# Kernel optimization log

Measured on AMD Instinct MI355X. Metric: run time of the kernel, lower is better.

Reference implementation:

```python
import jax, jax.numpy as jnp
import numpy as np
from math import pi

K_MAX = 0.1   # init k
DLT_K = 0.02  # init dk
EPS = 0.1

N_IMG, N_ATOM = 32, 400000


def _dot(a, b):
    # sum over last two dims, keepdims -> shape [..., 1, 1]
    return jnp.sum(a * b, axis=(-2, -1), keepdims=True)


def _norm(a):
    return jnp.sqrt(_dot(a, a))


def setup_inputs() -> dict:
    key = jax.random.key(0)
    k1, k2, k3 = jax.random.split(key, 3)
    pos = jax.random.normal(k1, (N_IMG, N_ATOM, 3), dtype=jnp.float32)
    frc = jax.random.normal(k2, (N_IMG, N_ATOM, 3), dtype=jnp.float32)
    eng = jax.random.normal(k3, (N_IMG,), dtype=jnp.float32)
    # ensure climbing-image argmax lies in the interior (valid frc_para index)
    eng = eng.at[N_IMG // 2].add(10.0)
    return {"pos": pos, "frc": frc, "eng": eng}


def reference(pos, frc, eng):
    dtype = pos.dtype
    eng3 = eng[:, None, None]  # [N,1,1]

    # ---- spring force k per segment: [N-1,1,1] ----
    eng_ref = jnp.min(eng3) - EPS
    eng_max = jnp.max(eng3)
    eng_i = jnp.maximum(eng3[1:], eng3[:-1])
    k = K_MAX - DLT_K * (eng_max - eng_i) / (eng_max - eng_ref)
    k = jnp.where(eng_i < eng_ref, K_MAX - DLT_K, k)

    # ---- improved tangent estimation: [N-2, A, 3] ----
    tau_p = pos[1:-1] - pos[:-2]
    tau_m = pos[2:] - pos[1:-1]
    e0, e1, e2 = eng3[:-2], eng3[1:-1], eng3[2:]
    msk_pp = ((e2 > e1) & (e1 > e0)).astype(dtype)
    msk_mm = ((e2 < e1) & (e1 < e0)).astype(dtype)
    not_both = 1.0 - jnp.maximum(msk_pp, msk_mm)
    msk_p = (e2 > e1).astype(dtype) * not_both
    msk_m = (e2 < e1).astype(dtype) * not_both
    dv_max = jnp.maximum(jnp.abs(e2 - e1), jnp.abs(e0 - e1))
    dv_min = jnp.minimum(jnp.abs(e2 - e1), jnp.abs(e0 - e1))
    tau = (tau_p * msk_pp + tau_m * msk_mm
           + (tau_p * dv_max + tau_m * dv_min) * msk_p
           + (tau_p * dv_min + tau_m * dv_max) * msk_m)
    tau = tau / _norm(tau)

    # ---- NEB force decomposition ----
    frc_in = frc[1:-1]
    vecp = pos[2:] - pos[1:-1]
    vecm = pos[1:-1] - pos[:-2]
    frc_para = _dot(frc_in, tau) * tau
    spr = k[1:] * vecp - k[:-1] * vecm
    spr_para = (k[1:] * _norm(vecp) - k[:-1] * _norm(vecm)) * tau
    frc_perp = frc_in - frc_para  # uses pre-climbing frc_para (torch in-place order)
    spr_perp = spr - spr_para

    # climbing image: double parallel force at the highest-energy image
    i = jnp.argmax(eng) - 1  # eng index -> frc_para index offset (interior images)
    # torch indexes frc_para with the raw eng argmax; reproduce that indexing
    i_raw = jnp.argmax(eng)
    frc_para = frc_para.at[i_raw].multiply(2.0)

    frc_neb = spr_para - frc_para  # nudged=True

    # doubly nudged switch term
    sw = (2.0 / pi) * jnp.arctan2(_dot(frc_perp, frc_perp), _dot(spr_perp, spr_perp))
    doubly = spr_perp - _dot(spr_perp, frc_perp) * frc_perp * sw
    frc_neb = frc_neb + doubly

    out_frc = frc + jnp.pad(frc_neb, ((1, 1), (0, 0), (0, 0)))
    return out_frc
```

## Files before the change

### kernel.cpp

```cpp
#include <hip/hip_runtime.h>
#include <math.h>

#define N_IMG 32
#define N_ATOM 400000
#define NE (N_ATOM*3)
#define NE4 (NE/4)
#define KMAXC 0.1f
#define DLTKC 0.02f
#define EPSE 0.1f

#define OFF_SDD 0
#define OFF_SPM 31
#define OFF_SFP 61
#define OFF_SFM 91
#define OFF_SFF 121
#define NSUM 151
#define OFF_CO 160

__device__ __forceinline__ float dot4(float4 a, float4 b) {
    return a.x*b.x + a.y*b.y + a.z*b.z + a.w*b.w;
}
__device__ __forceinline__ float4 sub4(float4 a, float4 b) {
    return make_float4(a.x-b.x, a.y-b.y, a.z-b.z, a.w-b.w);
}

__device__ __forceinline__ float wred_dpp(float x) {
    x += __int_as_float(__builtin_amdgcn_update_dpp(0, __float_as_int(x), 0x111, 0xf, 0xf, false));
    x += __int_as_float(__builtin_amdgcn_update_dpp(0, __float_as_int(x), 0x112, 0xf, 0xf, false));
    x += __int_as_float(__builtin_amdgcn_update_dpp(0, __float_as_int(x), 0x114, 0xf, 0xf, false));
    x += __int_as_float(__builtin_amdgcn_update_dpp(0, __float_as_int(x), 0x118, 0xf, 0xf, false));
    x += __int_as_float(__builtin_amdgcn_update_dpp(0, __float_as_int(x), 0x142, 0xa, 0xf, false));
    x += __int_as_float(__builtin_amdgcn_update_dpp(0, __float_as_int(x), 0x143, 0xc, 0xf, false));
    return x;
}

__global__ __launch_bounds__(256) void eb_pass1(const float* __restrict__ pos,
                                                const float* __restrict__ frc,
                                                float* __restrict__ sums) {
    __shared__ float ls[NSUM];
    for (int i = threadIdx.x; i < NSUM; i += 256) ls[i] = 0.f;
    __syncthreads();

    const int t = blockIdx.x * 256 + threadIdx.x;
    const bool act = t < NE4;
    const float4* pos4 = reinterpret_cast<const float4*>(pos);
    const float4* frc4 = reinterpret_cast<const float4*>(frc);
    const float4 z4 = make_float4(0.f, 0.f, 0.f, 0.f);
    const int lane = threadIdx.x & 63;

    float4 p0 = act ? pos4[t] : z4;
    float4 p1 = act ? pos4[(size_t)NE4 + t] : z4;
    float4 d_prev = sub4(p1, p0);
    {
        float sdd = wred_dpp(dot4(d_prev, d_prev));
        if (lane == 63) atomicAdd(&ls[OFF_SDD + 0], sdd);
    }
    float4 p_prev = p1;

#pragma unroll 5
    for (int r = 2; r < N_IMG; ++r) {
        float4 p = act ? pos4[(size_t)r * NE4 + t] : z4;
        float4 f = act ? frc4[(size_t)(r - 1) * NE4 + t] : z4;
        float4 d = sub4(p, p_prev);
        float sdd = wred_dpp(dot4(d, d));
        float spm = wred_dpp(dot4(d_prev, d));
        float sfp = wred_dpp(dot4(f, d_prev));
        float sfm = wred_dpp(dot4(f, d));
        float sff = wred_dpp(dot4(f, f));
        if (lane == 63) {
            int jj = r - 2;
            atomicAdd(&ls[OFF_SDD + (r - 1)], sdd);
            atomicAdd(&ls[OFF_SPM + jj], spm);
            atomicAdd(&ls[OFF_SFP + jj], sfp);
            atomicAdd(&ls[OFF_SFM + jj], sfm);
            atomicAdd(&ls[OFF_SFF + jj], sff);
        }
        p_prev = p;
        d_prev = d;
    }
    __syncthreads();
    for (int i = threadIdx.x; i < NSUM; i += 256) atomicAdd(&sums[i], ls[i]);
}

__global__ void eb_coeff(const float* __restrict__ eng,
                         const float* __restrict__ sums,
                         float* __restrict__ co) {
    const int jj = threadIdx.x;
    if (jj >= N_IMG - 2 || blockIdx.x != 0) return;
    float e[N_IMG];
    float emin = 1e30f, emax = -1e30f;
    int imax = 0;
    for (int i = 0; i < N_IMG; ++i) {
        float v = eng[i];
        e[i] = v;
        if (v < emin) emin = v;
        if (v > emax) { emax = v; imax = i; }
    }
    const float eref = emin - EPSE;
    float e0 = e[jj], e1 = e[jj + 1], e2 = e[jj + 2];
    float eim = fmaxf(e1, e0);
    float km = KMAXC - DLTKC * (emax - eim) / (emax - eref);
    if (eim < eref) km = KMAXC - DLTKC;
    float eip = fmaxf(e2, e1);
    float kp = KMAXC - DLTKC * (emax - eip) / (emax - eref);
    if (eip < eref) kp = KMAXC - DLTKC;

    float pp = (e2 > e1 && e1 > e0) ? 1.f : 0.f;
    float mm = (e2 < e1 && e1 < e0) ? 1.f : 0.f;
    float nb = 1.f - fmaxf(pp, mm);
    float mp = ((e2 > e1) ? 1.f : 0.f) * nb;
    float mq = ((e2 < e1) ? 1.f : 0.f) * nb;
    float dvmax = fmaxf(fabsf(e2 - e1), fabsf(e0 - e1));
    float dvmin = fminf(fabsf(e2 - e1), fabsf(e0 - e1));
    float a = pp + dvmax * mp + dvmin * mq;
    float b = mm + dvmin * mp + dvmax * mq;
    float Spp = sums[OFF_SDD + jj];
    float Smm = sums[OFF_SDD + jj + 1];
    float Spm = sums[OFF_SPM + jj];
    float Sfp = sums[OFF_SFP + jj];
    float Sfm = sums[OFF_SFM + jj];
    float Sff = sums[OFF_SFF + jj];
    float ntau2 = a * a * Spp + 2.f * a * b * Spm + b * b * Smm;
    float ntau = sqrtf(ntau2);
    float ta = a / ntau, tb = b / ntau;
    float fpar = ta * Sfp + tb * Sfm;
    float spar = kp * sqrtf(Smm) - km * sqrtf(Spp);
    float ffpp = Sff - fpar * fpar;
    float strau = ta * (kp * Spm - km * Spp) + tb * (kp * Smm - km * Spm);
    float Sss = kp * kp * Smm - 2.f * kp * km * Spm + km * km * Spp;
    float sspp = Sss - 2.f * spar * strau + spar * spar;
    float Ssf = kp * Sfm - km * Sfp;
    float spfp = Ssf - fpar * strau;
    float sw = (2.0f / 3.14159265358979323846f) * atan2f(ffpp, sspp);
    float c = spfp * sw;
    float g = (jj == imax) ? 2.f : 1.f;
    float w = (c - g) * fpar / ntau;
    co[jj]      = 1.f - c;
    co[30 + jj] = kp + w * b;
    co[60 + jj] = w * a - km;
}

__global__ __launch_bounds__(256) void eb_pass2(const float* __restrict__ pos,
                                                const float* __restrict__ frc,
                                                const float* __restrict__ co,
                                                float* __restrict__ out) {
    __shared__ float A[30], B[30], C[30];
    if (threadIdx.x < 30) {
        A[threadIdx.x] = co[threadIdx.x];
        B[threadIdx.x] = co[30 + threadIdx.x];
        C[threadIdx.x] = co[60 + threadIdx.x];
    }
    __syncthreads();
    const int t = blockIdx.x * 256 + threadIdx.x;
    if (t >= NE4) return;
    const float4* pos4 = reinterpret_cast<const float4*>(pos);
    const float4* frc4 = reinterpret_cast<const float4*>(frc);
    float4* out4 = reinterpret_cast<float4*>(out);

    size_t i31 = (size_t)31 * NE4 + t;
    float4 p_next = pos4[i31];
    out4[i31] = frc4[i31];
    float4 p30 = pos4[(size_t)30 * NE4 + t];
    float4 d_next = sub4(p_next, p30);
    p_next = p30;
#pragma unroll 5
    for (int l = 29; l >= 0; --l) {
        float4 p = pos4[(size_t)l * NE4 + t];
        float4 d = sub4(p_next, p);
        float4 f = frc4[(size_t)(l + 1) * NE4 + t];
        float ca = A[l], cb = B[l], cc = C[l];
        float4 o;
        o.x = ca * f.x + cb * d_next.x + cc * d.x;
        o.y = ca * f.y + cb * d_next.y + cc * d.y;
        o.z = ca * f.z + cb * d_next.z + cc * d.z;
        o.w = ca * f.w + cb * d_next.w + cc * d.w;
        out4[(size_t)(l + 1) * NE4 + t] = o;
        d_next = d;
        p_next = p;
    }
    out4[t] = frc4[t];
}

extern "C" void kernel_launch(void* const* d_in, const int* in_sizes, int n_in,
                              void* d_out, int out_size, void* d_ws, size_t ws_size,
                              hipStream_t stream) {
    const float* pos = (const float*)d_in[0];
    const float* frc = (const float*)d_in[1];
    const float* eng = (const float*)d_in[2];
    float* out = (float*)d_out;
    float* ws = (float*)d_ws;

    hipMemsetAsync(d_ws, 0, NSUM * sizeof(float), stream);
    const int blocks = (NE4 + 255) / 256;
    eb_pass1<<<blocks, 256, 0, stream>>>(pos, frc, ws);
    eb_coeff<<<1, 64, 0, stream>>>(eng, ws, ws + OFF_CO);
    eb_pass2<<<blocks, 256, 0, stream>>>(pos, frc, ws + OFF_CO, out);
}
```

Baseline: 440.3 us.

## Split image chain into chunks and replace atomic reductions with register partials

The first pass now splits the 30 interior images into 5 chunks spread over a 2D grid. Each thread grid-strides over elements and accumulates all dot-product sums in registers, so the per-image wave reductions and shared/global atomics are gone. Partial sums per block go to a workspace and a new reduce kernel combines them, which also removes the memset. The second pass is likewise chunked over images for more parallelism, at the cost of re-reading one boundary position image per chunk and one extra kernel launch.

```diff
diff --git a/kernel.cpp b/kernel.cpp
--- a/kernel.cpp
+++ b/kernel.cpp
@@ -15,7 +15,13 @@
 #define OFF_SFM 91
 #define OFF_SFF 121
 #define NSUM 151
-#define OFF_CO 160
+#define OFF_CO  160
+#define OFF_PART 256
+#define PSTRIDE 160
+
+#define NBXP 586
+#define NBX2 1172
+#define NCHUNK 5
 
 __device__ __forceinline__ float dot4(float4 a, float4 b) {
     return a.x*b.x + a.y*b.y + a.z*b.z + a.w*b.w;
@@ -36,50 +42,80 @@
 
 __global__ __launch_bounds__(256) void eb_pass1(const float* __restrict__ pos,
                                                 const float* __restrict__ frc,
-                                                float* __restrict__ sums) {
-    __shared__ float ls[NSUM];
-    for (int i = threadIdx.x; i < NSUM; i += 256) ls[i] = 0.f;
-    __syncthreads();
-
-    const int t = blockIdx.x * 256 + threadIdx.x;
-    const bool act = t < NE4;
+                                                float* __restrict__ part) {
+    const int c = blockIdx.y;
+    const int j0 = 1 + 6 * c;
     const float4* pos4 = reinterpret_cast<const float4*>(pos);
     const float4* frc4 = reinterpret_cast<const float4*>(frc);
-    const float4 z4 = make_float4(0.f, 0.f, 0.f, 0.f);
+
+    float sdd[7], spm[6], sfp[6], sfm[6], sff[6];
+#pragma unroll
+    for (int i = 0; i < 7; ++i) sdd[i] = 0.f;
+#pragma unroll
+    for (int i = 0; i < 6; ++i) { spm[i] = 0.f; sfp[i] = 0.f; sfm[i] = 0.f; sff[i] = 0.f; }
+
+    for (int t = blockIdx.x * 256 + threadIdx.x; t < NE4; t += 256 * NBXP) {
+        float4 p_cur = pos4[(size_t)(j0 - 1) * NE4 + t];
+        float4 p_nxt = pos4[(size_t)j0 * NE4 + t];
+        float4 dprev = sub4(p_nxt, p_cur);
+        sdd[0] += dot4(dprev, dprev);
+#pragma unroll
+        for (int jj = 0; jj < 6; ++jj) {
+            const int j = j0 + jj;
+            float4 p2 = pos4[(size_t)(j + 1) * NE4 + t];
+            float4 f  = frc4[(size_t)j * NE4 + t];
+            float4 d  = sub4(p2, p_nxt);
+            sdd[jj + 1] += dot4(d, d);
+            spm[jj] += dot4(dprev, d);
+            sfp[jj] += dot4(f, dprev);
+            sfm[jj] += dot4(f, d);
+            sff[jj] += dot4(f, f);
+            dprev = d;
+            p_nxt = p2;
+        }
+    }
+
+    float v[31];
+#pragma unroll
+    for (int i = 0; i < 7; ++i) v[i] = sdd[i];
+#pragma unroll
+    for (int i = 0; i < 6; ++i) { v[7 + i] = spm[i]; v[13 + i] = sfp[i]; v[19 + i] = sfm[i]; v[25 + i] = sff[i]; }
+
+    __shared__ float red[4][31];
+    const int wave = threadIdx.x >> 6;
     const int lane = threadIdx.x & 63;
-
-    float4 p0 = act ? pos4[t] : z4;
-    float4 p1 = act ? pos4[(size_t)NE4 + t] : z4;
-    float4 d_prev = sub4(p1, p0);
-    {
-        float sdd = wred_dpp(dot4(d_prev, d_prev));
-        if (lane == 63) atomicAdd(&ls[OFF_SDD + 0], sdd);
-    }
-    float4 p_prev = p1;
-
-#pragma unroll 5
-    for (int r = 2; r < N_IMG; ++r) {
-        float4 p = act ? pos4[(size_t)r * NE4 + t] : z4;
-        float4 f = act ? frc4[(size_t)(r - 1) * NE4 + t] : z4;
-        float4 d = sub4(p, p_prev);
-        float sdd = wred_dpp(dot4(d, d));
-        float spm = wred_dpp(dot4(d_prev, d));
-        float sfp = wred_dpp(dot4(f, d_prev));
-        float sfm = wred_dpp(dot4(f, d));
-        float sff = wred_dpp(dot4(f, f));
-        if (lane == 63) {
-            int jj = r - 2;
-            atomicAdd(&ls[OFF_SDD + (r - 1)], sdd);
-            atomicAdd(&ls[OFF_SPM + jj], spm);
-            atomicAdd(&ls[OFF_SFP + jj], sfp);
-            atomicAdd(&ls[OFF_SFM + jj], sfm);
-            atomicAdd(&ls[OFF_SFF + jj], sff);
-        }
-        p_prev = p;
-        d_prev = d;
+#pragma unroll
+    for (int s = 0; s < 31; ++s) {
+        float r = wred_dpp(v[s]);
+        if (lane == 63) red[wave][s] = r;
     }
     __syncthreads();
-    for (int i = threadIdx.x; i < NSUM; i += 256) atomicAdd(&sums[i], ls[i]);
+    const int s = threadIdx.x;
+    if (s < 31) {
+        float r = red[0][s] + red[1][s] + red[2][s] + red[3][s];
+        int slot; bool owned = true;
+        if (s < 7)       { owned = (s < 6) || (c == NCHUNK - 1); slot = OFF_SDD + (j0 - 1) + s; }
+        else if (s < 13) slot = OFF_SPM + (j0 - 1) + (s - 7);
+        else if (s < 19) slot = OFF_SFP + (j0 - 1) + (s - 13);
+        else if (s < 25) slot = OFF_SFM + (j0 - 1) + (s - 19);
+        else             slot = OFF_SFF + (j0 - 1) + (s - 25);
+        if (owned) part[(size_t)blockIdx.x * PSTRIDE + slot] = r;
+    }
+}
+
+__global__ __launch_bounds__(256) void eb_reduce(const float* __restrict__ part,
+                                                 float* __restrict__ sums) {
+    const int s = blockIdx.x;
+    float acc = 0.f;
+    for (int r = threadIdx.x; r < NBXP; r += 256)
+        acc += part[(size_t)r * PSTRIDE + s];
+    __shared__ float red[4];
+    const int wave = threadIdx.x >> 6;
+    const int lane = threadIdx.x & 63;
+    float v = wred_dpp(acc);
+    if (lane == 63) red[wave] = v;
+    __syncthreads();
+    if (threadIdx.x == 0) sums[s] = red[0] + red[1] + red[2] + red[3];
 }
 
 __global__ void eb_coeff(const float* __restrict__ eng,
@@ -132,10 +168,10 @@
     float Ssf = kp * Sfm - km * Sfp;
     float spfp = Ssf - fpar * strau;
     float sw = (2.0f / 3.14159265358979323846f) * atan2f(ffpp, sspp);
-    float c = spfp * sw;
+    float cc = spfp * sw;
     float g = (jj == imax) ? 2.f : 1.f;
-    float w = (c - g) * fpar / ntau;
-    co[jj]      = 1.f - c;
+    float w = (cc - g) * fpar / ntau;
+    co[jj]      = 1.f - cc;
     co[30 + jj] = kp + w * b;
     co[60 + jj] = w * a - km;
 }
@@ -153,32 +189,38 @@
     __syncthreads();
     const int t = blockIdx.x * 256 + threadIdx.x;
     if (t >= NE4) return;
+    const int c = blockIdx.y;
+    const int j0 = 1 + 6 * c;
     const float4* pos4 = reinterpret_cast<const float4*>(pos);
     const float4* frc4 = reinterpret_cast<const float4*>(frc);
     float4* out4 = reinterpret_cast<float4*>(out);
 
-    size_t i31 = (size_t)31 * NE4 + t;
-    float4 p_next = pos4[i31];
-    out4[i31] = frc4[i31];
-    float4 p30 = pos4[(size_t)30 * NE4 + t];
-    float4 d_next = sub4(p_next, p30);
-    p_next = p30;
-#pragma unroll 5
-    for (int l = 29; l >= 0; --l) {
-        float4 p = pos4[(size_t)l * NE4 + t];
-        float4 d = sub4(p_next, p);
-        float4 f = frc4[(size_t)(l + 1) * NE4 + t];
-        float ca = A[l], cb = B[l], cc = C[l];
+    if (c == 0) out4[t] = frc4[t];
+    if (c == NCHUNK - 1) {
+        size_t i31 = (size_t)31 * NE4 + t;
+        out4[i31] = frc4[i31];
+    }
+
+    float4 p_cur = pos4[(size_t)(j0 - 1) * NE4 + t];
+    float4 p_nxt = pos4[(size_t)j0 * NE4 + t];
+    float4 dprev = sub4(p_nxt, p_cur);
+#pragma unroll
+    for (int jj = 0; jj < 6; ++jj) {
+        const int j = j0 + jj;
+        float4 p2 = pos4[(size_t)(j + 1) * NE4 + t];
+        float4 f  = frc4[(size_t)j * NE4 + t];
+        float4 d  = sub4(p2, p_nxt);
+        const int g = j - 1;
+        float ca = A[g], cb = B[g], cd = C[g];
         float4 o;
-        o.x = ca * f.x + cb * d_next.x + cc * d.x;
-        o.y = ca * f.y + cb * d_next.y + cc * d.y;
-        o.z = ca * f.z + cb * d_next.z + cc * d.z;
-        o.w = ca * f.w + cb * d_next.w + cc * d.w;
-        out4[(size_t)(l + 1) * NE4 + t] = o;
-        d_next = d;
-        p_next = p;
-    }
-    out4[t] = frc4[t];
+        o.x = ca * f.x + cb * d.x + cd * dprev.x;
+        o.y = ca * f.y + cb * d.y + cd * dprev.y;
+        o.z = ca * f.z + cb * d.z + cd * dprev.z;
+        o.w = ca * f.w + cb * d.w + cd * dprev.w;
+        out4[(size_t)j * NE4 + t] = o;
+        dprev = d;
+        p_nxt = p2;
+    }
 }
 
 extern "C" void kernel_launch(void* const* d_in, const int* in_sizes, int n_in,
@@ -189,10 +231,12 @@
     const float* eng = (const float*)d_in[2];
     float* out = (float*)d_out;
     float* ws = (float*)d_ws;
-
-    hipMemsetAsync(d_ws, 0, NSUM * sizeof(float), stream);
-    const int blocks = (NE4 + 255) / 256;
-    eb_pass1<<<blocks, 256, 0, stream>>>(pos, frc, ws);
-    eb_coeff<<<1, 64, 0, stream>>>(eng, ws, ws + OFF_CO);
-    eb_pass2<<<blocks, 256, 0, stream>>>(pos, frc, ws + OFF_CO, out);
-}
+    float* sums = ws;
+    float* co   = ws + OFF_CO;
+    float* part = ws + OFF_PART;
+
+    eb_pass1<<<dim3(NBXP, NCHUNK), 256, 0, stream>>>(pos, frc, part);
+    eb_reduce<<<NSUM, 256, 0, stream>>>(part, sums);
+    eb_coeff<<<1, 64, 0, stream>>>(eng, sums, co);
+    eb_pass2<<<dim3(NBX2, NCHUNK), 256, 0, stream>>>(pos, frc, co, out);
+}
```

Result: faster. 421.6 us (-4.2%).
